# Performance work log

Measured on AMD Instinct MI355X. Metric: run time of the kernel, lower is better.

## Reference

```python
import jax, jax.numpy as jnp
import numpy as np

N_RAYS = 262144   # 512x512 rays
N_PTS = 128       # samples per ray (>= 50 required by depth-extraction loop)
FAR_DELTA = 1e10  # sentinel delta appended for the last sample


def setup_inputs() -> dict:
    key = jax.random.key(0)
    k1, k2, k3 = jax.random.split(key, 3)
    # sample_lengths along each ray are monotonically increasing -> sorted uniform in [2, 6)
    depth_values = jnp.sort(2.0 + 4.0 * jax.random.uniform(k1, (N_RAYS, N_PTS), dtype=jnp.float32), axis=1)
    # non-negative densities; uniform [0,1) so a good fraction exceed the 0.1 depth threshold
    density = jax.random.uniform(k2, (N_RAYS, N_PTS, 1), dtype=jnp.float32)
    feature = jax.random.uniform(k3, (N_RAYS, N_PTS, 3), dtype=jnp.float32)
    return {"depth_values": depth_values, "density": density, "feature": feature}


def reference(depth_values, density, feature):
    # deltas: successive depth differences, with a huge sentinel for the last sample
    deltas = jnp.concatenate(
        [depth_values[:, 1:] - depth_values[:, :-1],
         jnp.full_like(depth_values[:, :1], FAR_DELTA)], axis=1)[..., None]      # [N, P, 1]

    multiplier = jnp.exp(-deltas * density)                                      # [N, P, 1]
    # T[:, i] = prod_{k < i} multiplier[:, k]  (exclusive cumprod, T[:,0] = 1)
    T = jnp.concatenate(
        [jnp.ones_like(multiplier[:, :1]),
         jnp.cumprod(multiplier[:, :-1], axis=1)], axis=1)                       # [N, P, 1]
    weights = T * (1.0 - multiplier)                                             # [N, P, 1]

    feat = jnp.sum(weights * feature, axis=1)                                    # [N, 3]

    # Depth extraction: original loop sets depth = 1 - j/50 at the FIRST j in [0,50)
    # where density[:, j, 0] > 0.1 (later j's are blocked by depth >= 0.01).
    mask = density[:, :50, 0] > 0.1                                              # [N, 50]
    first_j = jnp.argmax(mask, axis=1)                                           # [N]
    hit = jnp.any(mask, axis=1)                                                  # [N]
    depth = jnp.where(hit, 1.0 - first_j.astype(jnp.float32) / 50.0, 0.0)[:, None]  # [N, 1]
    depth = depth / jnp.max(depth)

    return feat, depth
```

## Files before the change

kernel.cpp:

```cpp
#include <hip/hip_runtime.h>

#define NPTS 128
#define FAR_DELTA 1e10f

__global__ __launch_bounds__(256) void vr_main(
    const float* __restrict__ dv,
    const float* __restrict__ dens,
    const float* __restrict__ feat,
    float* __restrict__ out_feat,
    float* __restrict__ out_depth,
    int*   __restrict__ ws_max,
    int n_rays)
{
    const int lane = threadIdx.x & 63;
    const int wib  = threadIdx.x >> 6;
    const int wpb  = blockDim.x >> 6;
    const int gwave  = blockIdx.x * wpb + wib;
    const int nwaves = gridDim.x * wpb;

    float dmax = 0.0f;

    for (int ray = gwave; ray < n_rays; ray += nwaves) {
        const size_t rbase = (size_t)ray * NPTS;
        const float2 d2 = *(const float2*)(dv   + rbase + 2 * lane);
        const float2 s2 = *(const float2*)(dens + rbase + 2 * lane);
        const float2* fp = (const float2*)(feat + rbase * 3);
        const float2 f0 = fp[3 * lane + 0];
        const float2 f1 = fp[3 * lane + 1];
        const float2 f2 = fp[3 * lane + 2];

        const float d_next = __shfl_down(d2.x, 1);
        const float delta0 = d2.y - d2.x;
        const float delta1 = (lane == 63) ? FAR_DELTA : (d_next - d2.y);

        const float a0 = delta0 * s2.x;
        const float a1 = delta1 * s2.y;

        const float s_scan = (lane == 63) ? a0 : (a0 + a1);
        float pref = s_scan;
        #pragma unroll
        for (int off = 1; off < 64; off <<= 1) {
            const float t = __shfl_up(pref, off);
            if (lane >= off) pref += t;
        }
        const float excl = pref - s_scan;

        const float T0 = __expf(-excl);
        const float m0 = __expf(-a0);
        const float m1 = __expf(-a1);
        const float w0 = T0 * (1.0f - m0);
        const float w1 = T0 * m0 * (1.0f - m1);

        float c0 = w0 * f0.x + w1 * f1.y;
        float c1 = w0 * f0.y + w1 * f2.x;
        float c2 = w0 * f1.x + w1 * f2.y;

        #pragma unroll
        for (int off = 32; off >= 1; off >>= 1) {
            c0 += __shfl_down(c0, off);
            c1 += __shfl_down(c1, off);
            c2 += __shfl_down(c2, off);
        }

        const bool p0 = (lane < 25) && (s2.x > 0.1f);
        const bool p1 = (lane < 25) && (s2.y > 0.1f);
        const unsigned long long b0 = __ballot(p0);
        const unsigned long long b1 = __ballot(p1);
        const int j0 = b0 ? 2 * __builtin_ctzll(b0)     : 1000;
        const int j1 = b1 ? 2 * __builtin_ctzll(b1) + 1 : 1000;
        const int fj = min(j0, j1);
        const float draw = (fj < 50) ? (1.0f - (float)fj * 0.02f) : 0.0f;
        dmax = fmaxf(dmax, draw);

        if (lane == 0) {
            out_feat[(size_t)ray * 3 + 0] = c0;
            out_feat[(size_t)ray * 3 + 1] = c1;
            out_feat[(size_t)ray * 3 + 2] = c2;
            out_depth[ray] = draw;
        }
    }

    __shared__ float smax[8];
    if (lane == 0) smax[wib] = dmax;
    __syncthreads();
    if (threadIdx.x == 0) {
        float m = smax[0];
        for (int i = 1; i < wpb; ++i) m = fmaxf(m, smax[i]);
        atomicMax(ws_max, __float_as_int(m));
    }
}

__global__ __launch_bounds__(256) void vr_div(
    float* __restrict__ out_depth, const int* __restrict__ ws_max, int n)
{
    const int i = blockIdx.x * blockDim.x + threadIdx.x;
    const float mx = __int_as_float(*ws_max);
    if (i < n) out_depth[i] = out_depth[i] / mx;
}

extern "C" void kernel_launch(void* const* d_in, const int* in_sizes, int n_in,
                              void* d_out, int out_size, void* d_ws, size_t ws_size,
                              hipStream_t stream) {
    const float* dv   = (const float*)d_in[0];
    const float* dens = (const float*)d_in[1];
    const float* feat = (const float*)d_in[2];

    const int n_rays = in_sizes[0] / NPTS;

    float* out_feat  = (float*)d_out;
    float* out_depth = (float*)d_out + (size_t)n_rays * 3;
    int*   ws_max    = (int*)d_ws;

    hipMemsetAsync(ws_max, 0, sizeof(int), stream);

    const int threads = 256;
    const int blocks  = 2048;
    vr_main<<<blocks, threads, 0, stream>>>(dv, dens, feat, out_feat, out_depth,
                                            ws_max, n_rays);

    const int blocks2 = (n_rays + threads - 1) / threads;
    vr_div<<<blocks2, threads, 0, stream>>>(out_depth, ws_max, n_rays);
}
```

Before: 145.9 us.

## Process two rays per wavefront with float4 loads and vectorize depth normalization

```diff
diff --git a/kernel.cpp b/kernel.cpp
--- a/kernel.cpp
+++ b/kernel.cpp
@@ -13,66 +13,88 @@
     int n_rays)
 {
     const int lane = threadIdx.x & 63;
+    const int half = lane >> 5;
+    const int li   = lane & 31;
     const int wib  = threadIdx.x >> 6;
     const int wpb  = blockDim.x >> 6;
-    const int gwave  = blockIdx.x * wpb + wib;
-    const int nwaves = gridDim.x * wpb;
+    const int gwave   = blockIdx.x * wpb + wib;
+    const int nwaves  = gridDim.x * wpb;
+    const int n_pairs = (n_rays + 1) >> 1;
 
     float dmax = 0.0f;
 
-    for (int ray = gwave; ray < n_rays; ray += nwaves) {
-        const size_t rbase = (size_t)ray * NPTS;
-        const float2 d2 = *(const float2*)(dv   + rbase + 2 * lane);
-        const float2 s2 = *(const float2*)(dens + rbase + 2 * lane);
-        const float2* fp = (const float2*)(feat + rbase * 3);
-        const float2 f0 = fp[3 * lane + 0];
-        const float2 f1 = fp[3 * lane + 1];
-        const float2 f2 = fp[3 * lane + 2];
+    for (int pair = gwave; pair < n_pairs; pair += nwaves) {
+        const int ray_real = 2 * pair + half;
+        const int ray = min(ray_real, n_rays - 1);
+        const size_t pbase = (size_t)ray * NPTS + 4 * li;
+        const float4 d4 = *(const float4*)(dv   + pbase);
+        const float4 s4 = *(const float4*)(dens + pbase);
+        const float* fb = feat + (size_t)ray * (NPTS * 3) + 12 * li;
+        const float4 f0 = *(const float4*)(fb + 0);
+        const float4 f1 = *(const float4*)(fb + 4);
+        const float4 f2 = *(const float4*)(fb + 8);
 
-        const float d_next = __shfl_down(d2.x, 1);
-        const float delta0 = d2.y - d2.x;
-        const float delta1 = (lane == 63) ? FAR_DELTA : (d_next - d2.y);
+        const float dn = __shfl_down(d4.x, 1);
+        const float a0 = (d4.y - d4.x) * s4.x;
+        const float a1 = (d4.z - d4.y) * s4.y;
+        const float a2 = (d4.w - d4.z) * s4.z;
+        const float a3 = (li == 31) ? FAR_DELTA * s4.w : (dn - d4.w) * s4.w;
 
-        const float a0 = delta0 * s2.x;
-        const float a1 = delta1 * s2.y;
-
-        const float s_scan = (lane == 63) ? a0 : (a0 + a1);
+        const float s_scan = a0 + a1 + a2 + ((li == 31) ? 0.0f : a3);
         float pref = s_scan;
         #pragma unroll
-        for (int off = 1; off < 64; off <<= 1) {
+        for (int off = 1; off < 32; off <<= 1) {
             const float t = __shfl_up(pref, off);
-            if (lane >= off) pref += t;
+            if (li >= off) pref += t;
         }
         const float excl = pref - s_scan;
 
         const float T0 = __expf(-excl);
-        const float m0 = __expf(-a0);
-        const float m1 = __expf(-a1);
-        const float w0 = T0 * (1.0f - m0);
-        const float w1 = T0 * m0 * (1.0f - m1);
+        const float e0 = __expf(-a0);
+        const float e1 = __expf(-a1);
+        const float e2 = __expf(-a2);
+        const float e3 = __expf(-a3);
+        const float w0 = T0 * (1.0f - e0);
+        const float T1 = T0 * e0;
+        const float w1 = T1 * (1.0f - e1);
+        const float T2 = T1 * e1;
+        const float w2 = T2 * (1.0f - e2);
+        const float T3 = T2 * e2;
+        const float w3 = T3 * (1.0f - e3);
 
-        float c0 = w0 * f0.x + w1 * f1.y;
-        float c1 = w0 * f0.y + w1 * f2.x;
-        float c2 = w0 * f1.x + w1 * f2.y;
+        float c0 = w0 * f0.x + w1 * f0.w + w2 * f1.z + w3 * f2.y;
+        float c1 = w0 * f0.y + w1 * f1.x + w2 * f1.w + w3 * f2.z;
+        float c2 = w0 * f0.z + w1 * f1.y + w2 * f2.x + w3 * f2.w;
 
         #pragma unroll
-        for (int off = 32; off >= 1; off >>= 1) {
+        for (int off = 16; off >= 1; off >>= 1) {
             c0 += __shfl_down(c0, off);
             c1 += __shfl_down(c1, off);
             c2 += __shfl_down(c2, off);
         }
 
-        const bool p0 = (lane < 25) && (s2.x > 0.1f);
-        const bool p1 = (lane < 25) && (s2.y > 0.1f);
-        const unsigned long long b0 = __ballot(p0);
-        const unsigned long long b1 = __ballot(p1);
-        const int j0 = b0 ? 2 * __builtin_ctzll(b0)     : 1000;
-        const int j1 = b1 ? 2 * __builtin_ctzll(b1) + 1 : 1000;
-        const int fj = min(j0, j1);
-        const float draw = (fj < 50) ? (1.0f - (float)fj * 0.02f) : 0.0f;
+        const bool q0 = (li <= 12) && (s4.x > 0.1f);
+        const bool q1 = (li <= 12) && (s4.y > 0.1f);
+        const bool q2 = (li <= 11) && (s4.z > 0.1f);
+        const bool q3 = (li <= 11) && (s4.w > 0.1f);
+        const unsigned long long b0 = __ballot(q0);
+        const unsigned long long b1 = __ballot(q1);
+        const unsigned long long b2 = __ballot(q2);
+        const unsigned long long b3 = __ballot(q3);
+        const int sh = 32 * half;
+        const unsigned int m0 = (unsigned int)(b0 >> sh);
+        const unsigned int m1 = (unsigned int)(b1 >> sh);
+        const unsigned int m2 = (unsigned int)(b2 >> sh);
+        const unsigned int m3 = (unsigned int)(b3 >> sh);
+        int j = 1000;
+        if (m0) j = min(j, 4 * (int)__builtin_ctz(m0) + 0);
+        if (m1) j = min(j, 4 * (int)__builtin_ctz(m1) + 1);
+        if (m2) j = min(j, 4 * (int)__builtin_ctz(m2) + 2);
+        if (m3) j = min(j, 4 * (int)__builtin_ctz(m3) + 3);
+        const float draw = (j < 50) ? (1.0f - (float)j * 0.02f) : 0.0f;
         dmax = fmaxf(dmax, draw);
 
-        if (lane == 0) {
+        if (li == 0 && ray_real < n_rays) {
             out_feat[(size_t)ray * 3 + 0] = c0;
             out_feat[(size_t)ray * 3 + 1] = c1;
             out_feat[(size_t)ray * 3 + 2] = c2;
@@ -80,6 +102,7 @@
         }
     }
 
+    dmax = fmaxf(dmax, __shfl_xor(dmax, 32));
     __shared__ float smax[8];
     if (lane == 0) smax[wib] = dmax;
     __syncthreads();
@@ -93,9 +116,16 @@
 __global__ __launch_bounds__(256) void vr_div(
     float* __restrict__ out_depth, const int* __restrict__ ws_max, int n)
 {
-    const int i = blockIdx.x * blockDim.x + threadIdx.x;
-    const float mx = __int_as_float(*ws_max);
-    if (i < n) out_depth[i] = out_depth[i] / mx;
+    const int i4 = blockIdx.x * blockDim.x + threadIdx.x;
+    const float inv = 1.0f / __int_as_float(*ws_max);
+    const int n4 = n >> 2;
+    if (i4 < n4) {
+        float4 v = ((float4*)out_depth)[i4];
+        v.x *= inv; v.y *= inv; v.z *= inv; v.w *= inv;
+        ((float4*)out_depth)[i4] = v;
+    }
+    const int t = n4 * 4 + i4;
+    if (i4 < (n & 3) + 0 && t < n && (n & 3)) out_depth[t] *= inv;
 }
 
 extern "C" void kernel_launch(void* const* d_in, const int* in_sizes, int n_in,
@@ -118,6 +148,7 @@
     vr_main<<<blocks, threads, 0, stream>>>(dv, dens, feat, out_feat, out_depth,
                                             ws_max, n_rays);
 
-    const int blocks2 = (n_rays + threads - 1) / threads;
+    const int n4 = (n_rays + 3) / 4;
+    const int blocks2 = (n4 + threads - 1) / threads;
     vr_div<<<blocks2, threads, 0, stream>>>(out_depth, ws_max, n_rays);
 }
```

Result: faster. 137.5 us (-5.8%).
